# Kernel tuning notes

Measured on AMD Instinct MI355X. Metric: run time of the kernel, lower is better.

The kernel has to match this reference:

```python
import jax, jax.numpy as jnp
import numpy as np

N_NODES = 50000
N_EDGES = 800000
D = 128
SAME_W = 0.3
CROSS_W = 1.0


def setup_inputs() -> dict:
    key = jax.random.key(0)
    k1, k2, k3, k4, k5 = jax.random.split(key, 5)
    x = jax.random.normal(k1, (N_NODES, D), dtype=jnp.float32)
    edge_index = jax.random.randint(k2, (2, N_EDGES), 0, N_NODES, dtype=jnp.int64)
    edge_weight = jax.random.uniform(k3, (N_EDGES,), dtype=jnp.float32)
    Wr1 = jax.random.normal(k4, (D, D), dtype=jnp.float32) * (1.0 / np.sqrt(D))
    Wr2 = jax.random.normal(k5, (D, D), dtype=jnp.float32) * (1.0 / np.sqrt(D))
    return {"x": x, "edge_index": edge_index, "edge_weight": edge_weight,
            "Wr1": Wr1, "Wr2": Wr2, "cell_len": 20000}


def _node_types(idx, cell_len):
    # get_node_types: type 0 if idx <= cell_len, else 1 (note the <=, faithful to source)
    return (idx > cell_len).astype(jnp.int32)


def _conv_layer(x, src, dst, per_edge_w, Wr, n_nodes):
    # gather -> weight -> scatter-mean -> + root linear
    msg = x[src] * per_edge_w[:, None]                       # [E, D]
    agg = jax.ops.segment_sum(msg, dst, num_segments=n_nodes)  # [N, D]
    cnt = jax.ops.segment_sum(jnp.ones_like(per_edge_w), dst, num_segments=n_nodes)
    agg = agg / jnp.maximum(cnt, 1.0)[:, None]               # mean aggr (0 if no edges)
    return agg + x @ Wr.T                                     # lin_r, bias=False


def reference(x, edge_index, edge_weight, Wr1, Wr2, cell_len):
    src, dst = edge_index[0], edge_index[1]
    same = _node_types(src, cell_len) == _node_types(dst, cell_len)
    type_w = jnp.where(same, SAME_W, CROSS_W).astype(x.dtype)
    w = type_w * edge_weight                                  # [E]
    n_nodes = x.shape[0]
    h = _conv_layer(x, src, dst, w, Wr1, n_nodes)
    out = _conv_layer(h, src, dst, w, Wr2, n_nodes)
    return out
```

## Files before the change

### kernel.cpp

```cpp
#include <hip/hip_runtime.h>
#include <cstdint>
#include <cstddef>

#define D 128
#define SAME_W 0.3f
#define CROSS_W 1.0f
#define NSLICE 8
#define EPT 8
#define CAP 64
#define GEMM_BLOCKS 512

using bf16x8 = __attribute__((ext_vector_type(8))) __bf16;
using f32x4  = __attribute__((ext_vector_type(4))) float;

__device__ __forceinline__ unsigned bf16rne(float f) {
    unsigned u = __float_as_uint(f);
    return (u + 0x7FFFu + ((u >> 16) & 1u)) >> 16;
}

__global__ __launch_bounds__(256) void k_pre(
    const int* __restrict__ src, const int* __restrict__ dst,
    const float* __restrict__ ew, const int* __restrict__ cell_len,
    int* __restrict__ cnt, unsigned* __restrict__ meta, int E, int sliceLen,
    int nFill,
    const float4* __restrict__ x4, uint2* __restrict__ xh2,
    uint2* __restrict__ xl2, unsigned* __restrict__ xq, int nvec, int nSplit,
    const float* __restrict__ W1, const float* __restrict__ W2,
    unsigned* __restrict__ wsh, unsigned* __restrict__ w12h,
    unsigned* __restrict__ w12l)
{
    const int b = blockIdx.x;
    if (b < nFill) {
        const int slice = b & (NSLICE - 1);
        const int lo = slice * sliceLen, hi = lo + sliceLen;
        const int base = (b >> 3) * (256 * EPT) + threadIdx.x;
        const int c = *cell_len;
        #pragma unroll
        for (int u = 0; u < EPT; ++u) {
            int e = base + u * 256;
            if (e < E) {
                int d = __builtin_nontemporal_load(&dst[e]);
                if (d >= lo && d < hi) {
                    int s = __builtin_nontemporal_load(&src[e]);
                    float w = __builtin_nontemporal_load(&ew[e]);
                    float wt = w * (((s > c) == (d > c)) ? SAME_W : CROSS_W);
                    int pos = atomicAdd(&cnt[d], 1);
                    if (pos < CAP)
                        meta[d * CAP + pos] = (unsigned)s | (bf16rne(wt) << 16);
                }
            }
        }
    } else if (b < nFill + nSplit) {
        int i = (b - nFill) * 256 + threadIdx.x;
        if (i >= nvec) return;
        float4 v = x4[i];
        unsigned h0 = bf16rne(v.x), h1 = bf16rne(v.y),
                 h2 = bf16rne(v.z), h3 = bf16rne(v.w);
        xh2[i] = make_uint2(h0 | (h1 << 16), h2 | (h3 << 16));
        float r0 = v.x - __uint_as_float(h0 << 16);
        float r1 = v.y - __uint_as_float(h1 << 16);
        float r2 = v.z - __uint_as_float(h2 << 16);
        float r3 = v.w - __uint_as_float(h3 << 16);
        xl2[i] = make_uint2(bf16rne(r0) | (bf16rne(r1) << 16),
                            bf16rne(r2) | (bf16rne(r3) << 16));
        int q = __builtin_amdgcn_cvt_pk_fp8_f32(v.x, v.y, 0, false);
        q = __builtin_amdgcn_cvt_pk_fp8_f32(v.z, v.w, q, true);
        xq[i] = (unsigned)q;
    } else {
        int t = (b - nFill - nSplit) * 256 + threadIdx.x;
        int j = t >> 6, kp = t & 63;
        int k0 = kp * 2;
        float d0 = 0.f, d1 = 0.f;
        #pragma unroll 4
        for (int m = 0; m < D; ++m) {
            float a = W2[j * D + m];
            d0 = fmaf(a, W1[m * D + k0], d0);
            d1 = fmaf(a, W1[m * D + k0 + 1], d1);
        }
        float s0 = W1[j * D + k0] + W2[j * D + k0];
        float s1 = W1[j * D + k0 + 1] + W2[j * D + k0 + 1];
        wsh[j * 64 + kp] = bf16rne(s0) | (bf16rne(s1) << 16);
        unsigned h0 = bf16rne(d0), h1 = bf16rne(d1);
        w12h[j * 64 + kp] = h0 | (h1 << 16);
        float r0 = d0 - __uint_as_float(h0 << 16);
        float r1 = d1 - __uint_as_float(h1 << 16);
        w12l[j * 64 + kp] = bf16rne(r0) | (bf16rne(r1) << 16);
    }
}

template <bool EMIT_FP8>
__global__ __launch_bounds__(256) void k_agg_fp8(const unsigned short* __restrict__ xq,
                                                 const uint4* __restrict__ meta4,
                                                 const int* __restrict__ cnt,
                                                 unsigned* __restrict__ outb,
                                                 unsigned short* __restrict__ outq,
                                                 int N) {
    int gid = blockIdx.x * blockDim.x + threadIdx.x;
    int node = gid >> 6;
    int lane = gid & 63;
    if (node >= N) return;
    const int cn0 = cnt[node];
    const int cn = min(cn0, CAP);
    const uint4* mrow = meta4 + (size_t)node * (CAP / 4);
    float ax0 = 0.f, ay0 = 0.f, ax1 = 0.f, ay1 = 0.f;
    int i = 0;
    #pragma unroll 1
    for (; i + 16 <= cn; i += 16) {
        uint4 mq[4];
        #pragma unroll
        for (int u = 0; u < 4; ++u) mq[u] = mrow[(i >> 2) + u];
        unsigned short v[16];
        #pragma unroll
        for (int u = 0; u < 16; ++u) {
            unsigned m = ((const unsigned*)mq)[u];
            v[u] = xq[(size_t)(m & 0xFFFFu) * 64 + lane];
        }
        #pragma unroll
        for (int u = 0; u < 16; ++u) {
            unsigned m = ((const unsigned*)mq)[u];
            float wt = __uint_as_float(m & 0xFFFF0000u);
            float vx = __builtin_amdgcn_cvt_f32_fp8((unsigned)v[u], 0);
            float vy = __builtin_amdgcn_cvt_f32_fp8((unsigned)v[u], 1);
            if (u & 1) { ax1 = fmaf(vx, wt, ax1); ay1 = fmaf(vy, wt, ay1); }
            else       { ax0 = fmaf(vx, wt, ax0); ay0 = fmaf(vy, wt, ay0); }
        }
    }
    #pragma unroll 1
    for (; i + 4 <= cn; i += 4) {
        uint4 mq = mrow[i >> 2];
        unsigned short v[4];
        #pragma unroll
        for (int u = 0; u < 4; ++u)
            v[u] = xq[(size_t)(((const unsigned*)&mq)[u] & 0xFFFFu) * 64 + lane];
        #pragma unroll
        for (int u = 0; u < 4; ++u) {
            unsigned m = ((const unsigned*)&mq)[u];
            float wt = __uint_as_float(m & 0xFFFF0000u);
            float vx = __builtin_amdgcn_cvt_f32_fp8((unsigned)v[u], 0);
            float vy = __builtin_amdgcn_cvt_f32_fp8((unsigned)v[u], 1);
            if (u & 1) { ax1 = fmaf(vx, wt, ax1); ay1 = fmaf(vy, wt, ay1); }
            else       { ax0 = fmaf(vx, wt, ax0); ay0 = fmaf(vy, wt, ay0); }
        }
    }
    for (; i < cn; ++i) {
        unsigned m = ((const unsigned*)mrow)[i];
        float wt = __uint_as_float(m & 0xFFFF0000u);
        unsigned short v = xq[(size_t)(m & 0xFFFFu) * 64 + lane];
        ax0 = fmaf(__builtin_amdgcn_cvt_f32_fp8((unsigned)v, 0), wt, ax0);
        ay0 = fmaf(__builtin_amdgcn_cvt_f32_fp8((unsigned)v, 1), wt, ay0);
    }
    const float scale = 1.0f / (float)max(cn0, 1);
    const float rx = (ax0 + ax1) * scale, ry = (ay0 + ay1) * scale;
    outb[(size_t)node * 64 + lane] = bf16rne(rx) | (bf16rne(ry) << 16);
    if (EMIT_FP8) {
        int q = __builtin_amdgcn_cvt_pk_fp8_f32(rx, ry, 0, false);
        outq[(size_t)node * 64 + lane] = (unsigned short)(q & 0xFFFF);
    }
}

__global__ __launch_bounds__(256, 2) void k_gemm2(
    const uint4* __restrict__ xh4, const uint4* __restrict__ xl4,
    const uint4* __restrict__ a1h4,
    const uint4* __restrict__ w12h4, const uint4* __restrict__ w12l4,
    const uint4* __restrict__ wsh4,
    const unsigned* __restrict__ a2b,
    float* __restrict__ fout, int N, int nTiles)
{
    const int t = threadIdx.x;
    const int wave = t >> 6, lane = t & 63;
    const int j0 = wave * 32;
    const int lr = lane & 15;
    const int q  = lane >> 4;

    union FU { uint4 u; bf16x8 v; };

    FU wA[2][4], wB[2][4], wC[2][4];
    #pragma unroll
    for (int jt = 0; jt < 2; ++jt) {
        const int brow = (j0 + jt * 16 + lr) * 16 + q;
        #pragma unroll
        for (int ks = 0; ks < 4; ++ks) {
            wA[jt][ks].u = w12h4[brow + ks * 4];
            wB[jt][ks].u = w12l4[brow + ks * 4];
            wC[jt][ks].u = wsh4[brow + ks * 4];
        }
    }

#define LOAD_TILE(BX, BL, BA, BC, TILE) do {                                   \
    int row_ = (TILE) * 16 + lr; if (row_ > N - 1) row_ = N - 1;               \
    const int ar_ = row_ * 16 + q;                                             \
    _Pragma("unroll")                                                          \
    for (int ks = 0; ks < 4; ++ks) {                                           \
        BX[ks].u = xh4[ar_ + ks * 4];                                          \
        BL[ks].u = xl4[ar_ + ks * 4];                                          \
        BA[ks].u = a1h4[ar_ + ks * 4];                                         \
    }                                                                          \
    _Pragma("unroll")                                                          \
    for (int jt = 0; jt < 2; ++jt)                                             \
        _Pragma("unroll")                                                      \
        for (int r = 0; r < 4; ++r) {                                          \
            int rr_ = (TILE) * 16 + q * 4 + r; if (rr_ > N - 1) rr_ = N - 1;   \
            BC[jt * 4 + r] = a2b[(size_t)rr_ * 64 + ((j0 + jt * 16 + lr) >> 1)]; \
        }                                                                      \
} while (0)

#define COMPUTE_STORE(BX, BL, BA, BC, TILE) do {                               \
    f32x4 c_[2];                                                               \
    c_[0] = (f32x4){0.f, 0.f, 0.f, 0.f};                                       \
    c_[1] = (f32x4){0.f, 0.f, 0.f, 0.f};                                       \
    _Pragma("unroll")                                                          \
    for (int jt = 0; jt < 2; ++jt)                                             \
        _Pragma("unroll")                                                      \
        for (int ks = 0; ks < 4; ++ks) {                                       \
            c_[jt] = __builtin_amdgcn_mfma_f32_16x16x32_bf16(BX[ks].v, wA[jt][ks].v, c_[jt], 0, 0, 0); \
            c_[jt] = __builtin_amdgcn_mfma_f32_16x16x32_bf16(BL[ks].v, wA[jt][ks].v, c_[jt], 0, 0, 0); \
            c_[jt] = __builtin_amdgcn_mfma_f32_16x16x32_bf16(BX[ks].v, wB[jt][ks].v, c_[jt], 0, 0, 0); \
            c_[jt] = __builtin_amdgcn_mfma_f32_16x16x32_bf16(BA[ks].v, wC[jt][ks].v, c_[jt], 0, 0, 0); \
        }                                                                      \
    _Pragma("unroll")                                                          \
    for (int jt = 0; jt < 2; ++jt)                                             \
        _Pragma("unroll")                                                      \
        for (int r = 0; r < 4; ++r) {                                          \
            int rr_ = (TILE) * 16 + q * 4 + r;                                 \
            if (rr_ < N) {                                                     \
                unsigned w_ = BC[jt * 4 + r];                                  \
                float ci_ = __uint_as_float((lr & 1) ? (w_ & 0xFFFF0000u) : (w_ << 16)); \
                fout[(size_t)rr_ * D + j0 + jt * 16 + lr] = c_[jt][r] + ci_;   \
            }                                                                  \
        }                                                                      \
} while (0)

    FU Axh[4], Axl[4], Aa1[4]; unsigned Aci[8];
    FU Bxh[4], Bxl[4], Ba1[4]; unsigned Bci[8];

    int tile = blockIdx.x;
    const int step = gridDim.x;
    if (tile >= nTiles) return;
    LOAD_TILE(Axh, Axl, Aa1, Aci, tile);
    while (true) {
        int tn = tile + step;
        if (tn < nTiles) LOAD_TILE(Bxh, Bxl, Ba1, Bci, tn);
        COMPUTE_STORE(Axh, Axl, Aa1, Aci, tile);
        tile = tn;
        if (tile >= nTiles) break;
        tn = tile + step;
        if (tn < nTiles) LOAD_TILE(Axh, Axl, Aa1, Aci, tn);
        COMPUTE_STORE(Bxh, Bxl, Ba1, Bci, tile);
        tile = tn;
        if (tile >= nTiles) break;
    }
#undef LOAD_TILE
#undef COMPUTE_STORE
}

extern "C" void kernel_launch(void* const* d_in, const int* in_sizes, int n_in,
                              void* d_out, int out_size, void* d_ws, size_t ws_size,
                              hipStream_t stream) {
    const float* x        = (const float*)d_in[0];
    const int*   ei       = (const int*)d_in[1];
    const float* ew       = (const float*)d_in[2];
    const float* Wr1      = (const float*)d_in[3];
    const float* Wr2      = (const float*)d_in[4];
    const int*   cell_len = (const int*)d_in[5];

    const int N = in_sizes[0] / D;
    const int E = in_sizes[1] / 2;
    const int* src = ei;
    const int* dst = ei + E;

    char* ws = (char*)d_ws;
    size_t off = 0;
    unsigned* meta = (unsigned*)(ws + off); off += (size_t)4 * CAP * N;
    int*      cnt  = (int*)     (ws + off); off += (size_t)4 * N;
    off = (off + 255) & ~(size_t)255;
    unsigned* xh   = (unsigned*)(ws + off); off += (size_t)2 * N * D;
    unsigned* xl   = (unsigned*)(ws + off); off += (size_t)2 * N * D;
    unsigned* a1h  = (unsigned*)(ws + off); off += (size_t)2 * N * D;
    unsigned* a2b  = (unsigned*)(ws + off); off += (size_t)2 * N * D;
    unsigned* xq   = (unsigned*)(ws + off); off += (size_t)1 * N * D;
    unsigned* a1q  = (unsigned*)(ws + off); off += (size_t)1 * N * D;
    unsigned* wsh  = (unsigned*)(ws + off); off += (size_t)2 * D * D;
    unsigned* w12h = (unsigned*)(ws + off); off += (size_t)2 * D * D;
    unsigned* w12l = (unsigned*)(ws + off); off += (size_t)2 * D * D;
    if (ws_size < off) return;
    float* out = (float*)d_out;

    hipMemsetAsync(cnt, 0, (size_t)4 * N, stream);

    const int sliceLen = (N + NSLICE - 1) / NSLICE;
    const int nFill  = ((E + 256 * EPT - 1) / (256 * EPT)) * NSLICE;
    const int xvec   = N * D / 4;
    const int nSplit = (xvec + 255) / 256;
    const int nW     = (D * 64 + 255) / 256;
    const int aggBlocks = (N + 3) / 4;
    const int nTiles = (N + 15) / 16;

    k_pre<<<nFill + nSplit + nW, 256, 0, stream>>>(
        src, dst, ew, cell_len, cnt, meta, E, sliceLen, nFill,
        (const float4*)x, (uint2*)xh, (uint2*)xl, xq, xvec, nSplit,
        Wr1, Wr2, wsh, w12h, w12l);

    k_agg_fp8<true ><<<aggBlocks, 256, 0, stream>>>(
        (const unsigned short*)xq, (const uint4*)meta, cnt,
        a1h, (unsigned short*)a1q, N);
    k_agg_fp8<false><<<aggBlocks, 256, 0, stream>>>(
        (const unsigned short*)a1q, (const uint4*)meta, cnt,
        a2b, nullptr, N);

    k_gemm2<<<GEMM_BLOCKS, 256, 0, stream>>>((const uint4*)xh, (const uint4*)xl,
                                             (const uint4*)a1h,
                                             (const uint4*)w12h, (const uint4*)w12l,
                                             (const uint4*)wsh, a2b, out, N, nTiles);
}
```

Measured before the change: 225.4 us.

## Bucket edges by destination slice before scattering into per-node adjacency

Edge preprocessing is split into two passes. First, each block reads its edges once and appends packed (dst, src, weight) entries into per-slice buckets using shared-memory counters, which replaces eight redundant slice passes over the edge arrays. A new scatter kernel then walks each slice bucket and does the per-node atomic insert into the CAP-sized adjacency, keeping atomics localized to one slice. This adds an extra kernel launch and an intermediate buffer round trip. It also packs dst and src into 16 bits each, which only holds while the node count stays below 65536, and it caps each slice at SLAB entries.

New measurement: 227.2 us. About the same (+0.8%).

```diff
diff --git a/kernel.cpp b/kernel.cpp
--- a/kernel.cpp
+++ b/kernel.cpp
@@ -6,8 +6,9 @@
 #define SAME_W 0.3f
 #define CROSS_W 1.0f
 #define NSLICE 8
-#define EPT 8
 #define CAP 64
+#define P1_EPT 8
+#define SLAB 131072
 #define GEMM_BLOCKS 512
 
 using bf16x8 = __attribute__((ext_vector_type(8))) __bf16;
@@ -21,8 +22,8 @@
 __global__ __launch_bounds__(256) void k_pre(
     const int* __restrict__ src, const int* __restrict__ dst,
     const float* __restrict__ ew, const int* __restrict__ cell_len,
-    int* __restrict__ cnt, unsigned* __restrict__ meta, int E, int sliceLen,
-    int nFill,
+    int* __restrict__ scnt, uint2* __restrict__ ebuf, int E, int sliceLen,
+    int nFillC,
     const float4* __restrict__ x4, uint2* __restrict__ xh2,
     uint2* __restrict__ xl2, unsigned* __restrict__ xq, int nvec, int nSplit,
     const float* __restrict__ W1, const float* __restrict__ W2,
@@ -30,28 +31,45 @@
     unsigned* __restrict__ w12l)
 {
     const int b = blockIdx.x;
-    if (b < nFill) {
-        const int slice = b & (NSLICE - 1);
-        const int lo = slice * sliceLen, hi = lo + sliceLen;
-        const int base = (b >> 3) * (256 * EPT) + threadIdx.x;
+    if (b < nFillC) {
+        __shared__ int lcnt[NSLICE];
+        __shared__ int lbase[NSLICE];
+        const int t = threadIdx.x;
+        if (t < NSLICE) lcnt[t] = 0;
+        __syncthreads();
         const int c = *cell_len;
-        #pragma unroll
-        for (int u = 0; u < EPT; ++u) {
+        const int base = b * (256 * P1_EPT) + t;
+        int   sl[P1_EPT], rk[P1_EPT];
+        uint2 en[P1_EPT];
+        #pragma unroll
+        for (int u = 0; u < P1_EPT; ++u) {
             int e = base + u * 256;
+            sl[u] = -1;
             if (e < E) {
                 int d = __builtin_nontemporal_load(&dst[e]);
-                if (d >= lo && d < hi) {
-                    int s = __builtin_nontemporal_load(&src[e]);
-                    float w = __builtin_nontemporal_load(&ew[e]);
-                    float wt = w * (((s > c) == (d > c)) ? SAME_W : CROSS_W);
-                    int pos = atomicAdd(&cnt[d], 1);
-                    if (pos < CAP)
-                        meta[d * CAP + pos] = (unsigned)s | (bf16rne(wt) << 16);
-                }
+                int s = __builtin_nontemporal_load(&src[e]);
+                float w = __builtin_nontemporal_load(&ew[e]);
+                float wt = w * (((s > c) == (d > c)) ? SAME_W : CROSS_W);
+                int slice = d / sliceLen;
+                sl[u] = slice;
+                en[u].x = (unsigned)d | ((unsigned)s << 16);
+                en[u].y = bf16rne(wt);
+                rk[u] = atomicAdd(&lcnt[slice], 1);
             }
         }
-    } else if (b < nFill + nSplit) {
-        int i = (b - nFill) * 256 + threadIdx.x;
+        __syncthreads();
+        if (t < NSLICE) lbase[t] = atomicAdd(&scnt[t], lcnt[t]);
+        __syncthreads();
+        #pragma unroll
+        for (int u = 0; u < P1_EPT; ++u) {
+            if (sl[u] >= 0) {
+                int idx = lbase[sl[u]] + rk[u];
+                if (idx < SLAB)
+                    ebuf[(size_t)sl[u] * SLAB + idx] = en[u];
+            }
+        }
+    } else if (b < nFillC + nSplit) {
+        int i = (b - nFillC) * 256 + threadIdx.x;
         if (i >= nvec) return;
         float4 v = x4[i];
         unsigned h0 = bf16rne(v.x), h1 = bf16rne(v.y),
@@ -67,7 +85,7 @@
         q = __builtin_amdgcn_cvt_pk_fp8_f32(v.z, v.w, q, true);
         xq[i] = (unsigned)q;
     } else {
-        int t = (b - nFill - nSplit) * 256 + threadIdx.x;
+        int t = (b - nFillC - nSplit) * 256 + threadIdx.x;
         int j = t >> 6, kp = t & 63;
         int k0 = kp * 2;
         float d0 = 0.f, d1 = 0.f;
@@ -85,6 +103,24 @@
         float r0 = d0 - __uint_as_float(h0 << 16);
         float r1 = d1 - __uint_as_float(h1 << 16);
         w12l[j * 64 + kp] = bf16rne(r0) | (bf16rne(r1) << 16);
+    }
+}
+
+__global__ __launch_bounds__(256) void k_scatter(const uint2* __restrict__ ebuf,
+                                                 const int* __restrict__ scnt,
+                                                 int* __restrict__ cnt,
+                                                 unsigned* __restrict__ meta) {
+    const int s = blockIdx.x & (NSLICE - 1);
+    const int chunk = blockIdx.x >> 3;
+    const int n = min(scnt[s], SLAB);
+    const uint2* buf = ebuf + (size_t)s * SLAB;
+    const int step = (GEMM_BLOCKS / NSLICE) * 256;
+    for (int i = chunk * 256 + threadIdx.x; i < n; i += step) {
+        uint2 en = buf[i];
+        int d = en.x & 0xFFFFu;
+        unsigned mw = (en.x >> 16) | (en.y << 16);
+        int pos = atomicAdd(&cnt[d], 1);
+        if (pos < CAP) meta[d * CAP + pos] = mw;
     }
 }
 
@@ -272,7 +308,9 @@
     size_t off = 0;
     unsigned* meta = (unsigned*)(ws + off); off += (size_t)4 * CAP * N;
     int*      cnt  = (int*)     (ws + off); off += (size_t)4 * N;
+    int*      scnt = (int*)     (ws + off); off += (size_t)4 * NSLICE;
     off = (off + 255) & ~(size_t)255;
+    uint2*    ebuf = (uint2*)   (ws + off); off += (size_t)8 * SLAB * NSLICE;
     unsigned* xh   = (unsigned*)(ws + off); off += (size_t)2 * N * D;
     unsigned* xl   = (unsigned*)(ws + off); off += (size_t)2 * N * D;
     unsigned* a1h  = (unsigned*)(ws + off); off += (size_t)2 * N * D;
@@ -285,20 +323,22 @@
     if (ws_size < off) return;
     float* out = (float*)d_out;
 
-    hipMemsetAsync(cnt, 0, (size_t)4 * N, stream);
+    hipMemsetAsync(cnt, 0, (size_t)4 * (N + NSLICE), stream);
 
     const int sliceLen = (N + NSLICE - 1) / NSLICE;
-    const int nFill  = ((E + 256 * EPT - 1) / (256 * EPT)) * NSLICE;
+    const int nFillC = (E + 256 * P1_EPT - 1) / (256 * P1_EPT);
     const int xvec   = N * D / 4;
     const int nSplit = (xvec + 255) / 256;
     const int nW     = (D * 64 + 255) / 256;
     const int aggBlocks = (N + 3) / 4;
     const int nTiles = (N + 15) / 16;
 
-    k_pre<<<nFill + nSplit + nW, 256, 0, stream>>>(
-        src, dst, ew, cell_len, cnt, meta, E, sliceLen, nFill,
+    k_pre<<<nFillC + nSplit + nW, 256, 0, stream>>>(
+        src, dst, ew, cell_len, scnt, ebuf, E, sliceLen, nFillC,
         (const float4*)x, (uint2*)xh, (uint2*)xl, xq, xvec, nSplit,
         Wr1, Wr2, wsh, w12h, w12l);
+
+    k_scatter<<<GEMM_BLOCKS, 256, 0, stream>>>(ebuf, scnt, cnt, meta);
 
     k_agg_fp8<true ><<<aggBlocks, 256, 0, stream>>>(
         (const unsigned short*)xq, (const uint4*)meta, cnt,
```
